# Optimization experiments

Hardware: AMD Instinct MI355X
Metric: run time of the kernel (lower is better)

The kernel has to match this reference:

```python
import jax, jax.numpy as jnp
import numpy as np

B, T, D = 2, 2048, 2048
H, HD, RD = 16, 192, 64
CD = HD - RD          # 128 content dims per head
QR, DL = 768, 512     # q lora rank, kv latent dim
THETA = 10000.0


def setup_inputs() -> dict:
    key = jax.random.key(0)
    ks = jax.random.split(key, 9)
    s = 0.02
    return {
        "x": jax.random.normal(ks[0], (B, T, D), jnp.float32),
        "wq_down": jax.random.normal(ks[1], (D, QR), jnp.float32) * s,
        "wq_up": jax.random.normal(ks[2], (QR, H * CD), jnp.float32) * s,
        "wq_rope": jax.random.normal(ks[3], (D, H * RD), jnp.float32) * s,
        "wkv_down": jax.random.normal(ks[4], (D, DL), jnp.float32) * s,
        "wk_up": jax.random.normal(ks[5], (DL, H * CD), jnp.float32) * s,
        "wv_up": jax.random.normal(ks[6], (DL, H * HD), jnp.float32) * s,
        "wk_rope": jax.random.normal(ks[7], (D, H * RD), jnp.float32) * s,
        "wo": jax.random.normal(ks[8], (H * HD, D), jnp.float32) * s,
    }


def _rope_tables(seq_len):
    inv = 1.0 / (THETA ** (jnp.arange(0, RD, 2, dtype=jnp.float32) / RD))  # [RD/2]
    ang = jnp.arange(seq_len, dtype=jnp.float32)[:, None] * inv[None, :]  # [T, RD/2]
    return jnp.cos(ang), jnp.sin(ang)


def _apply_rope(x, cos, sin):
    # x: [B,H,T,RD]; cos/sin: [T,RD/2] broadcast over B,H
    d = RD // 2
    x1, x2 = x[..., :d], x[..., d:]
    return jnp.concatenate([x1 * cos - x2 * sin, x1 * sin + x2 * cos], axis=-1)


def reference(x, wq_down, wq_up, wq_rope, wkv_down, wk_up, wv_up, wk_rope, wo):
    # projections
    q_c = (x @ wq_down) @ wq_up                       # [B,T,H*CD]
    q_p = x @ wq_rope                                 # [B,T,H*RD]
    latent = x @ wkv_down                             # [B,T,DL]
    k_c = latent @ wk_up                              # [B,T,H*CD]
    k_p = x @ wk_rope                                 # [B,T,H*RD]
    v = latent @ wv_up                                # [B,T,H*HD]

    def heads(t, d):
        return t.reshape(B, T, H, d).transpose(0, 2, 1, 3)  # [B,H,T,d]

    q_c, q_p = heads(q_c, CD), heads(q_p, RD)
    k_c, k_p = heads(k_c, CD), heads(k_p, RD)
    v = heads(v, HD)

    cos, sin = _rope_tables(T)
    q_p = _apply_rope(q_p, cos, sin)
    k_p = _apply_rope(k_p, cos, sin)

    q = jnp.concatenate([q_c, q_p], axis=-1)          # [B,H,T,HD]
    k = jnp.concatenate([k_c, k_p], axis=-1)          # [B,H,T,HD]

    scale = 1.0 / jnp.sqrt(jnp.asarray(HD, q.dtype))
    scores = jnp.einsum("bhqd,bhkd->bhqk", q, k) * scale
    causal = jnp.tril(jnp.ones((T, T), dtype=bool))
    scores = jnp.where(causal, scores, jnp.finfo(scores.dtype).min)
    attn = jax.nn.softmax(scores, axis=-1)
    out = jnp.einsum("bhqk,bhkd->bhqd", attn, v)      # [B,H,T,HD]
    out = out.transpose(0, 2, 1, 3).reshape(B, T, H * HD)
    return out @ wo                                   # [B,T,D]
```

## Files before the change

### kernel.cpp

```cpp
#include <hip/hip_runtime.h>
#include <hip/hip_bf16.h>
#include <cstdint>
#include <cstddef>

typedef __bf16 bf16_t;
typedef __bf16 bf16x8 __attribute__((ext_vector_type(8)));
typedef float f32x4 __attribute__((ext_vector_type(4)));

#define MFMA16(a, b, c) __builtin_amdgcn_mfma_f32_16x16x32_bf16((a), (b), (c), 0, 0, 0)

__device__ __forceinline__ void gload_lds16(const void* g, void* l) {
  __builtin_amdgcn_global_load_lds((__attribute__((address_space(1))) void*)(g),
                                   (__attribute__((address_space(3))) void*)(l),
                                   16, 0, 0);
}

__device__ __forceinline__ uint32_t pkbf(float lo, float hi) {
  union { bf16_t h[2]; uint32_t u; } u2;
  u2.h[0] = (bf16_t)lo; u2.h[1] = (bf16_t)hi;
  return u2.u;
}

__global__ __launch_bounds__(256) void cvt_f32_to_bf16(const float* __restrict__ in,
                                                       bf16_t* __restrict__ out) {
  size_t i = ((size_t)blockIdx.x * 256 + threadIdx.x) * 4;
  float4 v = *(const float4*)(in + i);
  bf16_t o[4] = {(bf16_t)v.x, (bf16_t)v.y, (bf16_t)v.z, (bf16_t)v.w};
  *(uint2*)(out + i) = *(uint2*)o;
}

__global__ __launch_bounds__(256) void transpose_w(const float* __restrict__ in,
                                                   bf16_t* __restrict__ out, int R, int C) {
  __shared__ bf16_t tile[32][33];
  int c0 = blockIdx.x * 32, r0 = blockIdx.y * 32;
  int tx = threadIdx.x, ty = threadIdx.y;
#pragma unroll
  for (int s = 0; s < 4; s++) {
    int r = ty + s * 8;
    tile[r][tx] = (bf16_t)in[(size_t)(r0 + r) * C + c0 + tx];
  }
  __syncthreads();
#pragma unroll
  for (int s = 0; s < 4; s++) {
    int r = ty + s * 8;
    out[(size_t)(c0 + r) * R + r0 + tx] = tile[tx][r];
  }
}

__global__ __launch_bounds__(256) void transpose_v_kernel(const bf16_t* __restrict__ v,
                                                          bf16_t* __restrict__ vt) {
  __shared__ bf16_t tile[32][33];
  int bh = blockIdx.z;
  int t0 = blockIdx.x * 32, d0 = blockIdx.y * 32;
  int tx = threadIdx.x, ty = threadIdx.y;
  const bf16_t* src = v + (size_t)(bh >> 4) * 2048 * 3072 + (bh & 15) * 192;
#pragma unroll
  for (int s = 0; s < 4; s++) {
    int t = ty + s * 8;
    tile[t][tx] = src[(size_t)(t0 + t) * 3072 + d0 + tx];
  }
  __syncthreads();
  bf16_t* dst = vt + (size_t)bh * 192 * 2048;
#pragma unroll
  for (int s = 0; s < 4; s++) {
    int d = ty + s * 8;
    dst[(size_t)(d0 + d) * 2048 + t0 + tx] = tile[tx][d];
  }
}

__global__ __launch_bounds__(256) void rope_inplace(bf16_t* __restrict__ buf) {
  int idx = blockIdx.x * 256 + threadIdx.x;
  int j = idx & 31;
  int h = (idx >> 5) & 15;
  int row = idx >> 9;
  int t = row & 2047;
  size_t base = (size_t)row * 3072 + h * 192 + 128;
  float inv = expf(-(float)j * 0.28782313662425574f);
  float ang = (float)t * inv;
  float c, s;
  sincosf(ang, &s, &c);
  float x1 = (float)buf[base + j];
  float x2 = (float)buf[base + j + 32];
  buf[base + j]      = (bf16_t)(x1 * c - x2 * s);
  buf[base + j + 32] = (bf16_t)(x1 * s + x2 * c);
}

template <int MODE>
__global__ __launch_bounds__(512, 2) void gemm_bt2(const bf16_t* __restrict__ A, int lda,
                                                   const bf16_t* __restrict__ Bt,
                                                   void* __restrict__ C0, void* __restrict__ C1,
                                                   void* __restrict__ C2, int K, int ldc) {
  __shared__ __align__(16) bf16_t sA0[256 * 64];
  __shared__ __align__(16) bf16_t sB0[128 * 64];
  __shared__ __align__(16) bf16_t sA1[256 * 64];
  __shared__ __align__(16) bf16_t sB1[128 * 64];
  const int tid = threadIdx.x;
  const int l = tid & 63, w = tid >> 6;
  const int l15 = l & 15, l4 = (l >> 4) & 3;
  const int wr = w >> 1, wc = w & 1;
  const int m0 = blockIdx.y * 256, n0 = blockIdx.x * 128;
  const int nt = K >> 6;

  f32x4 acc[4][4] = {};

#define STAGEG(SA, SB, KT)                                                          \
  {                                                                                 \
    const int kts = (KT) * 64;                                                      \
    _Pragma("unroll")                                                               \
    for (int r = 0; r < 4; r++) {                                                   \
      int i = r * 512 + tid;                                                        \
      int row = i >> 3, cl = i & 7;                                                 \
      int cg = cl ^ (row & 7);                                                      \
      gload_lds16(A + (size_t)(m0 + row) * lda + kts + cg * 8,                      \
                  (char*)(SA) + (size_t)(r * 512 + w * 64) * 16);                   \
    }                                                                               \
    _Pragma("unroll")                                                               \
    for (int r = 0; r < 2; r++) {                                                   \
      int i = r * 512 + tid;                                                        \
      int row = i >> 3, cl = i & 7;                                                 \
      int cg = cl ^ (row & 7);                                                      \
      gload_lds16(Bt + (size_t)(n0 + row) * K + kts + cg * 8,                       \
                  (char*)(SB) + (size_t)(r * 512 + w * 64) * 16);                   \
    }                                                                               \
  }

#define GCOMPUTE(SA, SB)                                                            \
  {                                                                                 \
    _Pragma("unroll")                                                               \
    for (int ks = 0; ks < 2; ks++) {                                                \
      bf16x8 af[4], bfr[4];                                                         \
      _Pragma("unroll")                                                             \
      for (int mf = 0; mf < 4; mf++) {                                              \
        int row = wr * 64 + mf * 16 + l15;                                          \
        int cl = (ks * 4 + l4) ^ (row & 7);                                         \
        af[mf] = *(const bf16x8*)((SA) + row * 64 + cl * 8);                        \
      }                                                                             \
      _Pragma("unroll")                                                             \
      for (int nf = 0; nf < 4; nf++) {                                              \
        int row = wc * 64 + nf * 16 + l15;                                          \
        int cl = (ks * 4 + l4) ^ (row & 7);                                         \
        bfr[nf] = *(const bf16x8*)((SB) + row * 64 + cl * 8);                       \
      }                                                                             \
      _Pragma("unroll")                                                             \
      for (int mf = 0; mf < 4; mf++)                                                \
        _Pragma("unroll")                                                           \
        for (int nf = 0; nf < 4; nf++)                                              \
          acc[mf][nf] = MFMA16(af[mf], bfr[nf], acc[mf][nf]);                       \
    }                                                                               \
  }

  STAGEG(sA0, sB0, 0)
  for (int t = 0; t < nt; t += 2) {
    STAGEG(sA1, sB1, t + 1)
    asm volatile("s_waitcnt vmcnt(6)\n\ts_barrier" ::: "memory");
    GCOMPUTE(sA0, sB0)
    asm volatile("s_barrier" ::: "memory");
    if (t + 2 < nt) {
      STAGEG(sA0, sB0, t + 2)
      asm volatile("s_waitcnt vmcnt(6)\n\ts_barrier" ::: "memory");
    } else {
      asm volatile("s_waitcnt vmcnt(0)\n\ts_barrier" ::: "memory");
    }
    GCOMPUTE(sA1, sB1)
    asm volatile("s_barrier" ::: "memory");
  }
#undef STAGEG
#undef GCOMPUTE

#pragma unroll
  for (int mf = 0; mf < 4; mf++)
#pragma unroll
    for (int nf = 0; nf < 4; nf++)
#pragma unroll
      for (int r = 0; r < 4; r++) {
        int m = m0 + wr * 64 + mf * 16 + l4 * 4 + r;
        int n = n0 + wc * 64 + nf * 16 + l15;
        float v = acc[mf][nf][r];
        if constexpr (MODE == 1) {
          ((float*)C0)[(size_t)m * ldc + n] = v;
        } else if constexpr (MODE == 2) {
          ((bf16_t*)C0)[(size_t)m * 3072 + (n >> 7) * 192 + (n & 127)] = (bf16_t)v;
        } else if constexpr (MODE == 4) {
          if (n < 1280) {
            ((bf16_t*)C0)[(size_t)m * 1280 + n] = (bf16_t)v;
          } else if (n < 2304) {
            int nn = n - 1280;
            ((bf16_t*)C1)[(size_t)m * 3072 + (nn >> 6) * 192 + 128 + (nn & 63)] = (bf16_t)v;
          } else {
            int nn = n - 2304;
            ((bf16_t*)C2)[(size_t)m * 3072 + (nn >> 6) * 192 + 128 + (nn & 63)] = (bf16_t)v;
          }
        } else {
          if (n < 2048) {
            ((bf16_t*)C0)[(size_t)m * 3072 + (n >> 7) * 192 + (n & 127)] = (bf16_t)v;
          } else {
            ((bf16_t*)C1)[(size_t)m * 3072 + (n - 2048)] = (bf16_t)v;
          }
        }
      }
}

__global__ __launch_bounds__(512, 2) void attn_kernel(const bf16_t* __restrict__ q,
                                                      const bf16_t* __restrict__ kbuf,
                                                      const bf16_t* __restrict__ vt,
                                                      bf16_t* __restrict__ ao) {
  __shared__ __align__(16) bf16_t sK0[64][192];
  __shared__ __align__(16) bf16_t sK1[64][192];
  __shared__ __align__(16) bf16_t sV0[192][64];
  __shared__ __align__(16) bf16_t sV1[192][64];

  const int tid = threadIdx.x, l = tid & 63, w = tid >> 6;
  const int l15 = l & 15, l4 = (l >> 4) & 3;
  const int bh = blockIdx.x & 31;
  const int c = blockIdx.x >> 5;
  const int b = bh >> 4, h = bh & 15;
  const int ca = c, cb = 15 - c;
  const int ra = ca * 128 + w * 16;
  const int rb = cb * 128 + w * 16;
  const int tga = 2 * ca + (w >> 2);
  const int tgb = 2 * cb + (w >> 2);

  const bf16_t* qp = q + (size_t)b * 2048 * 3072 + h * 192;
  const bf16_t* kp = kbuf + (size_t)b * 2048 * 3072 + h * 192;
  const bf16_t* vp = vt + (size_t)bh * 192 * 2048;

  bf16x8 qf[2][6];
#pragma unroll
  for (int kd = 0; kd < 6; kd++) {
    qf[0][kd] = *(const bf16x8*)(qp + (size_t)(ra + l15) * 3072 + kd * 32 + l4 * 8);
    qf[1][kd] = *(const bf16x8*)(qp + (size_t)(rb + l15) * 3072 + kd * 32 + l4 * 8);
  }

  f32x4 o[2][12] = {};
  float mrow[2] = {-__builtin_inff(), -__builtin_inff()};
  float lrow[2] = {0.0f, 0.0f};

  const float scale = 0.07216878364870322f;
  const float THR = 7.0f;
  const int nkt = 2 * cb + 2;
  const int src0 = l15 + ((l4 & 1) << 5);
  const int src1 = src0 + 16;
  const bool hibank = (l4 & 2) != 0;

#define STAGE(SK, SV, KT)                                                           \
  {                                                                                 \
    const int k0s = (KT) * 64;                                                      \
    _Pragma("unroll")                                                               \
    for (int r = 0; r < 3; r++) {                                                   \
      int i = r * 512 + tid;                                                        \
      int row = i / 24, cc = i % 24;                                                \
      int g = cc - (row & 7) * 3;                                                   \
      if (g < 0) g += 24;                                                           \
      gload_lds16(kp + (size_t)(k0s + row) * 3072 + g * 8,                          \
                  (char*)&SK[0][0] + (size_t)(r * 512 + w * 64) * 16);              \
    }                                                                               \
    _Pragma("unroll")                                                               \
    for (int r = 0; r < 3; r++) {                                                   \
      int i = r * 512 + tid;                                                        \
      int d = i >> 3, cc = i & 7;                                                   \
      gload_lds16(vp + (size_t)d * 2048 + k0s + (cc ^ (d & 7)) * 8,                 \
                  (char*)&SV[0][0] + (size_t)(r * 512 + w * 64) * 16);              \
    }                                                                               \
  }

#define SOFTMAX_CHUNK(c, rbase, tg)                                                    \
    {                                                                                  \
      const bool diag = (kt == (tg));                                                  \
      _Pragma("unroll")                                                                \
      for (int nf = 0; nf < 4; nf++)                                                   \
        _Pragma("unroll")                                                              \
        for (int r = 0; r < 4; r++) {                                                  \
          float sv = s[c][nf][r] * scale;                                              \
          if (diag) {                                                                  \
            int ktok = k0 + nf * 16 + l4 * 4 + r;                                      \
            if (ktok > (rbase) + l15) sv = -__builtin_inff();                          \
          }                                                                            \
          s[c][nf][r] = sv;                                                            \
        }                                                                              \
      float m_in = s[c][0][0];                                                         \
      _Pragma("unroll")                                                                \
      for (int nf = 0; nf < 4; nf++)                                                   \
        _Pragma("unroll")                                                              \
        for (int r = 0; r < 4; r++)                                                    \
          if (nf | r) m_in = fmaxf(m_in, s[c][nf][r]);                                 \
      m_in = fmaxf(m_in, __shfl_xor(m_in, 16));                                        \
      m_in = fmaxf(m_in, __shfl_xor(m_in, 32));                                        \
      if (!__all(m_in - mrow[c] <= THR)) {                                             \
        float mn = fmaxf(mrow[c], m_in);                                               \
        float alpha = __expf(mrow[c] - mn);                                            \
        mrow[c] = mn;                                                                  \
        lrow[c] *= alpha;                                                              \
        f32x4 av;                                                                      \
        _Pragma("unroll")                                                              \
        for (int r = 0; r < 4; r++) av[r] = __shfl(alpha, l4 * 4 + r);                 \
        _Pragma("unroll")                                                              \
        for (int nf2 = 0; nf2 < 12; nf2++) o[c][nf2] *= av;                            \
      }                                                                                \
      float rs = 0.0f;                                                                 \
      _Pragma("unroll")                                                                \
      for (int nf = 0; nf < 4; nf++)                                                   \
        _Pragma("unroll")                                                              \
        for (int r = 0; r < 4; r++) {                                                  \
          float pv = __expf(s[c][nf][r] - mrow[c]);                                    \
          s[c][nf][r] = pv;                                                            \
          rs += pv;                                                                    \
        }                                                                              \
      rs += __shfl_xor(rs, 16);                                                        \
      rs += __shfl_xor(rs, 32);                                                        \
      lrow[c] += rs;                                                                   \
      uint32_t wq[8];                                                                  \
      _Pragma("unroll")                                                                \
      for (int nf = 0; nf < 4; nf++) {                                                 \
        wq[nf * 2 + 0] = pkbf(s[c][nf][0], s[c][nf][1]);                               \
        wq[nf * 2 + 1] = pkbf(s[c][nf][2], s[c][nf][3]);                               \
      }                                                                                \
      _Pragma("unroll")                                                                \
      for (int ks = 0; ks < 2; ks++) {                                                 \
        uint32_t A0 = __shfl(wq[(2 * ks) * 2 + 0], src0);                              \
        uint32_t A1 = __shfl(wq[(2 * ks) * 2 + 1], src0);                              \
        uint32_t B0 = __shfl(wq[(2 * ks + 1) * 2 + 0], src0);                          \
        uint32_t B1 = __shfl(wq[(2 * ks + 1) * 2 + 1], src0);                          \
        uint32_t C0w = __shfl(wq[(2 * ks) * 2 + 0], src1);                             \
        uint32_t C1w = __shfl(wq[(2 * ks) * 2 + 1], src1);                             \
        uint32_t D0 = __shfl(wq[(2 * ks + 1) * 2 + 0], src1);                          \
        uint32_t D1 = __shfl(wq[(2 * ks + 1) * 2 + 1], src1);                          \
        union { uint32_t u[4]; bf16x8 v; } fr;                                         \
        fr.u[0] = hibank ? B0 : A0;                                                    \
        fr.u[1] = hibank ? B1 : A1;                                                    \
        fr.u[2] = hibank ? D0 : C0w;                                                   \
        fr.u[3] = hibank ? D1 : C1w;                                                   \
        pa[c][ks] = fr.v;                                                              \
      }                                                                                \
    }

#define TILE_BODY(SK, SV, KT)                                                          \
  {                                                                                    \
    const int kt = (KT);                                                               \
    const int k0 = kt * 64;                                                            \
    const bool act_a = (kt <= tga);                                                    \
    const bool act_b = (kt <= tgb);                                                    \
    f32x4 s[2][4] = {};                                                                \
    _Pragma("unroll")                                                                  \
    for (int kd = 0; kd < 6; kd++) {                                                   \
      bf16x8 bk[4];                                                                    \
      _Pragma("unroll")                                                                \
      for (int nf = 0; nf < 4; nf++) {                                                 \
        int row = nf * 16 + l15;                                                       \
        int cl = kd * 4 + l4 + (row & 7) * 3;                                          \
        if (cl >= 24) cl -= 24;                                                        \
        bk[nf] = *(const bf16x8*)(&SK[row][cl * 8]);                                   \
      }                                                                                \
      if (act_b) {                                                                     \
        _Pragma("unroll")                                                              \
        for (int nf = 0; nf < 4; nf++)                                                 \
          s[1][nf] = MFMA16(bk[nf], qf[1][kd], s[1][nf]);                              \
      }                                                                                \
      if (act_a) {                                                                     \
        _Pragma("unroll")                                                              \
        for (int nf = 0; nf < 4; nf++)                                                 \
          s[0][nf] = MFMA16(bk[nf], qf[0][kd], s[0][nf]);                              \
      }                                                                                \
    }                                                                                  \
    bf16x8 pa[2][2] = {};                                                              \
    if (act_b) SOFTMAX_CHUNK(1, rb, tgb)                                               \
    if (act_a) SOFTMAX_CHUNK(0, ra, tga)                                               \
    _Pragma("unroll")                                                                  \
    for (int ks = 0; ks < 2; ks++) {                                                   \
      _Pragma("unroll")                                                                \
      for (int nf2 = 0; nf2 < 12; nf2++) {                                             \
        int d = nf2 * 16 + l15;                                                        \
        int cl = (ks * 4 + l4) ^ (d & 7);                                              \
        bf16x8 vb = *(const bf16x8*)(&SV[d][cl * 8]);                                  \
        if (act_b) o[1][nf2] = MFMA16(pa[1][ks], vb, o[1][nf2]);                       \
        if (act_a) o[0][nf2] = MFMA16(pa[0][ks], vb, o[0][nf2]);                       \
      }                                                                                \
    }                                                                                  \
  }

  STAGE(sK0, sV0, 0)
  __syncthreads();

  for (int kt0 = 0; kt0 < nkt; kt0 += 2) {
    STAGE(sK1, sV1, kt0 + 1)
    TILE_BODY(sK0, sV0, kt0)
    __syncthreads();
    if (kt0 + 2 < nkt) STAGE(sK0, sV0, kt0 + 2)
    TILE_BODY(sK1, sV1, kt0 + 1)
    __syncthreads();
  }
#undef STAGE
#undef SOFTMAX_CHUNK
#undef TILE_BODY

#pragma unroll
  for (int mf = 0; mf < 2; mf++) {
    const int rbase = (mf == 0) ? ra : rb;
#pragma unroll
    for (int r = 0; r < 4; r++) {
      float lv = __shfl(lrow[mf], l4 * 4 + r);
      float inv = 1.0f / lv;
      int qrow = rbase + l4 * 4 + r;
#pragma unroll
      for (int nf2 = 0; nf2 < 12; nf2++) {
        int d = nf2 * 16 + l15;
        ao[(size_t)(b * 2048 + qrow) * 3072 + h * 192 + d] = (bf16_t)(o[mf][nf2][r] * inv);
      }
    }
  }
}

extern "C" void kernel_launch(void* const* d_in, const int* in_sizes, int n_in,
                              void* d_out, int out_size, void* d_ws, size_t ws_size,
                              hipStream_t stream) {
  const float* x       = (const float*)d_in[0];
  const float* wq_down = (const float*)d_in[1];
  const float* wq_up   = (const float*)d_in[2];
  const float* wq_rope = (const float*)d_in[3];
  const float* wkv_down= (const float*)d_in[4];
  const float* wk_up   = (const float*)d_in[5];
  const float* wv_up   = (const float*)d_in[6];
  const float* wk_rope = (const float*)d_in[7];
  const float* wo      = (const float*)d_in[8];
  float* out = (float*)d_out;

  char* p = (char*)d_ws;
  auto take = [&](size_t elems) { bf16_t* r = (bf16_t*)p; p += elems * 2; return r; };
  bf16_t* xb    = take(4096ull * 2048);
  bf16_t* fw1   = take(3328ull * 2048);
  bf16_t* wqu_t = take(2048ull * 768);
  bf16_t* fw2   = take(5120ull * 512);
  bf16_t* wo_t  = take(2048ull * 3072);
  bf16_t* qkvd  = take(4096ull * 1280);
  bf16_t* qbuf  = take(4096ull * 3072);
  bf16_t* kbuf  = take(4096ull * 3072);
  bf16_t* vbuf  = take(4096ull * 3072);
  bf16_t* vt    = take(4096ull * 3072);
  bf16_t* ao    = vbuf;

  dim3 tb(32, 8);
  cvt_f32_to_bf16<<<8192, 256, 0, stream>>>(x, xb);
  transpose_w<<<dim3(24, 64), tb, 0, stream>>>(wq_down,  fw1,                 2048, 768);
  transpose_w<<<dim3(16, 64), tb, 0, stream>>>(wkv_down, fw1 + 768ull * 2048, 2048, 512);
  transpose_w<<<dim3(32, 64), tb, 0, stream>>>(wq_rope,  fw1 + 1280ull * 2048,2048, 1024);
  transpose_w<<<dim3(32, 64), tb, 0, stream>>>(wk_rope,  fw1 + 2304ull * 2048,2048, 1024);
  transpose_w<<<dim3(64, 24), tb, 0, stream>>>(wq_up,    wqu_t,               768, 2048);
  transpose_w<<<dim3(64, 16), tb, 0, stream>>>(wk_up,    fw2,                 512, 2048);
  transpose_w<<<dim3(96, 16), tb, 0, stream>>>(wv_up,    fw2 + 2048ull * 512, 512, 3072);
  transpose_w<<<dim3(64, 96), tb, 0, stream>>>(wo,       wo_t,                3072, 2048);

  gemm_bt2<4><<<dim3(26, 16), 512, 0, stream>>>(xb, 2048, fw1, qkvd, qbuf, kbuf, 2048, 0);
  gemm_bt2<2><<<dim3(16, 16), 512, 0, stream>>>(qkvd, 1280, wqu_t, qbuf, nullptr, nullptr, 768, 0);
  gemm_bt2<5><<<dim3(40, 16), 512, 0, stream>>>(qkvd + 768, 1280, fw2, kbuf, vbuf, nullptr, 512, 0);

  rope_inplace<<<8192, 256, 0, stream>>>(qbuf);
  rope_inplace<<<8192, 256, 0, stream>>>(kbuf);
  transpose_v_kernel<<<dim3(64, 6, 32), tb, 0, stream>>>(vbuf, vt);

  attn_kernel<<<256, 512, 0, stream>>>(qbuf, kbuf, vt, ao);

  gemm_bt2<1><<<dim3(16, 16), 512, 0, stream>>>(ao, 3072, wo_t, out, nullptr, nullptr, 3072, 2048);
}
```

Measured before the change: 373.3 us.

## Fuse weight transposes, rope launches, and write V transposed from GEMM epilogue

Merges the eight weight-transpose launches into one flat-grid kernel and the two rope launches into one. The K/V up-projection GEMM epilogue now writes V directly in per-head transposed layout using packed 4-element stores, which removes the separate V transpose kernel and its extra pass over V. This cuts launch overhead and memory traffic. The trade-off is a more complex epilogue with strided stores across the T dimension.

```diff
diff --git a/kernel.cpp b/kernel.cpp
--- a/kernel.cpp
+++ b/kernel.cpp
@@ -29,47 +29,45 @@
   *(uint2*)(out + i) = *(uint2*)o;
 }
 
-__global__ __launch_bounds__(256) void transpose_w(const float* __restrict__ in,
-                                                   bf16_t* __restrict__ out, int R, int C) {
+__global__ __launch_bounds__(256) void transpose_all(
+    const float* __restrict__ s0, const float* __restrict__ s1,
+    const float* __restrict__ s2, const float* __restrict__ s3,
+    const float* __restrict__ s4, const float* __restrict__ s5,
+    const float* __restrict__ s6, const float* __restrict__ s7,
+    bf16_t* __restrict__ t0, bf16_t* __restrict__ t1, bf16_t* __restrict__ t2,
+    bf16_t* __restrict__ t3, bf16_t* __restrict__ t4, bf16_t* __restrict__ t5,
+    bf16_t* __restrict__ t6, bf16_t* __restrict__ t7) {
   __shared__ bf16_t tile[32][33];
-  int c0 = blockIdx.x * 32, r0 = blockIdx.y * 32;
-  int tx = threadIdx.x, ty = threadIdx.y;
+  const int lid = blockIdx.x;
+  const float* src; bf16_t* dst; int R, C, bx, by;
+  if (lid < 1536)       { src=s0; dst=t0; R=2048; C=768;  int lo=lid;        bx=lo%24; by=lo/24; }
+  else if (lid < 2560)  { src=s1; dst=t1; R=2048; C=512;  int lo=lid-1536;   bx=lo%16; by=lo/16; }
+  else if (lid < 4608)  { src=s2; dst=t2; R=2048; C=1024; int lo=lid-2560;   bx=lo%32; by=lo/32; }
+  else if (lid < 6656)  { src=s3; dst=t3; R=2048; C=1024; int lo=lid-4608;   bx=lo%32; by=lo/32; }
+  else if (lid < 8192)  { src=s4; dst=t4; R=768;  C=2048; int lo=lid-6656;   bx=lo%64; by=lo/64; }
+  else if (lid < 9216)  { src=s5; dst=t5; R=512;  C=2048; int lo=lid-8192;   bx=lo%64; by=lo/64; }
+  else if (lid < 10752) { src=s6; dst=t6; R=512;  C=3072; int lo=lid-9216;   bx=lo%96; by=lo/96; }
+  else                  { src=s7; dst=t7; R=3072; C=2048; int lo=lid-10752;  bx=lo%64; by=lo/64; }
+  const int c0 = bx * 32, r0 = by * 32;
+  const int tx = threadIdx.x, ty = threadIdx.y;
 #pragma unroll
   for (int s = 0; s < 4; s++) {
     int r = ty + s * 8;
-    tile[r][tx] = (bf16_t)in[(size_t)(r0 + r) * C + c0 + tx];
+    tile[r][tx] = (bf16_t)src[(size_t)(r0 + r) * C + c0 + tx];
   }
   __syncthreads();
 #pragma unroll
   for (int s = 0; s < 4; s++) {
     int r = ty + s * 8;
-    out[(size_t)(c0 + r) * R + r0 + tx] = tile[tx][r];
-  }
-}
-
-__global__ __launch_bounds__(256) void transpose_v_kernel(const bf16_t* __restrict__ v,
-                                                          bf16_t* __restrict__ vt) {
-  __shared__ bf16_t tile[32][33];
-  int bh = blockIdx.z;
-  int t0 = blockIdx.x * 32, d0 = blockIdx.y * 32;
-  int tx = threadIdx.x, ty = threadIdx.y;
-  const bf16_t* src = v + (size_t)(bh >> 4) * 2048 * 3072 + (bh & 15) * 192;
-#pragma unroll
-  for (int s = 0; s < 4; s++) {
-    int t = ty + s * 8;
-    tile[t][tx] = src[(size_t)(t0 + t) * 3072 + d0 + tx];
-  }
-  __syncthreads();
-  bf16_t* dst = vt + (size_t)bh * 192 * 2048;
-#pragma unroll
-  for (int s = 0; s < 4; s++) {
-    int d = ty + s * 8;
-    dst[(size_t)(d0 + d) * 2048 + t0 + tx] = tile[tx][d];
-  }
-}
-
-__global__ __launch_bounds__(256) void rope_inplace(bf16_t* __restrict__ buf) {
-  int idx = blockIdx.x * 256 + threadIdx.x;
+    dst[(size_t)(c0 + r) * R + r0 + tx] = tile[tx][r];
+  }
+}
+
+__global__ __launch_bounds__(256) void rope_both(bf16_t* __restrict__ qb,
+                                                 bf16_t* __restrict__ kb) {
+  const int gid = blockIdx.x;
+  bf16_t* buf = (gid < 8192) ? qb : kb;
+  int idx = (gid & 8191) * 256 + threadIdx.x;
   int j = idx & 31;
   int h = (idx >> 5) & 15;
   int row = idx >> 9;
@@ -170,34 +168,53 @@
 #pragma unroll
   for (int mf = 0; mf < 4; mf++)
 #pragma unroll
-    for (int nf = 0; nf < 4; nf++)
-#pragma unroll
-      for (int r = 0; r < 4; r++) {
-        int m = m0 + wr * 64 + mf * 16 + l4 * 4 + r;
-        int n = n0 + wc * 64 + nf * 16 + l15;
-        float v = acc[mf][nf][r];
-        if constexpr (MODE == 1) {
-          ((float*)C0)[(size_t)m * ldc + n] = v;
-        } else if constexpr (MODE == 2) {
-          ((bf16_t*)C0)[(size_t)m * 3072 + (n >> 7) * 192 + (n & 127)] = (bf16_t)v;
-        } else if constexpr (MODE == 4) {
-          if (n < 1280) {
-            ((bf16_t*)C0)[(size_t)m * 1280 + n] = (bf16_t)v;
-          } else if (n < 2304) {
-            int nn = n - 1280;
-            ((bf16_t*)C1)[(size_t)m * 3072 + (nn >> 6) * 192 + 128 + (nn & 63)] = (bf16_t)v;
-          } else {
-            int nn = n - 2304;
-            ((bf16_t*)C2)[(size_t)m * 3072 + (nn >> 6) * 192 + 128 + (nn & 63)] = (bf16_t)v;
-          }
+    for (int nf = 0; nf < 4; nf++) {
+      const int mbase = m0 + wr * 64 + mf * 16 + l4 * 4;
+      const int n = n0 + wc * 64 + nf * 16 + l15;
+      if constexpr (MODE == 1) {
+#pragma unroll
+        for (int r = 0; r < 4; r++)
+          ((float*)C0)[(size_t)(mbase + r) * ldc + n] = acc[mf][nf][r];
+      } else if constexpr (MODE == 2) {
+#pragma unroll
+        for (int r = 0; r < 4; r++)
+          ((bf16_t*)C0)[(size_t)(mbase + r) * 3072 + (n >> 7) * 192 + (n & 127)] =
+              (bf16_t)acc[mf][nf][r];
+      } else if constexpr (MODE == 4) {
+        if (n < 1280) {
+#pragma unroll
+          for (int r = 0; r < 4; r++)
+            ((bf16_t*)C0)[(size_t)(mbase + r) * 1280 + n] = (bf16_t)acc[mf][nf][r];
+        } else if (n < 2304) {
+          int nn = n - 1280;
+#pragma unroll
+          for (int r = 0; r < 4; r++)
+            ((bf16_t*)C1)[(size_t)(mbase + r) * 3072 + (nn >> 6) * 192 + 128 + (nn & 63)] =
+                (bf16_t)acc[mf][nf][r];
         } else {
-          if (n < 2048) {
-            ((bf16_t*)C0)[(size_t)m * 3072 + (n >> 7) * 192 + (n & 127)] = (bf16_t)v;
-          } else {
-            ((bf16_t*)C1)[(size_t)m * 3072 + (n - 2048)] = (bf16_t)v;
-          }
+          int nn = n - 2304;
+#pragma unroll
+          for (int r = 0; r < 4; r++)
+            ((bf16_t*)C2)[(size_t)(mbase + r) * 3072 + (nn >> 6) * 192 + 128 + (nn & 63)] =
+                (bf16_t)acc[mf][nf][r];
+        }
+      } else {
+        if (n < 2048) {
+#pragma unroll
+          for (int r = 0; r < 4; r++)
+            ((bf16_t*)C0)[(size_t)(mbase + r) * 3072 + (n >> 7) * 192 + (n & 127)] =
+                (bf16_t)acc[mf][nf][r];
+        } else {
+          int nn = n - 2048;
+          int hh = nn / 192, dd = nn - hh * 192;
+          int bb = mbase >> 11, tt = mbase & 2047;
+          bf16_t pk4[4] = {(bf16_t)acc[mf][nf][0], (bf16_t)acc[mf][nf][1],
+                           (bf16_t)acc[mf][nf][2], (bf16_t)acc[mf][nf][3]};
+          *(uint2*)((bf16_t*)C1 + ((size_t)(bb * 16 + hh) * 192 + dd) * 2048 + tt) =
+              *(uint2*)pk4;
         }
       }
+    }
 }
 
 __global__ __launch_bounds__(512, 2) void attn_kernel(const bf16_t* __restrict__ q,
@@ -433,28 +450,21 @@
   bf16_t* qkvd  = take(4096ull * 1280);
   bf16_t* qbuf  = take(4096ull * 3072);
   bf16_t* kbuf  = take(4096ull * 3072);
-  bf16_t* vbuf  = take(4096ull * 3072);
+  bf16_t* ao    = take(4096ull * 3072);
   bf16_t* vt    = take(4096ull * 3072);
-  bf16_t* ao    = vbuf;
 
   dim3 tb(32, 8);
   cvt_f32_to_bf16<<<8192, 256, 0, stream>>>(x, xb);
-  transpose_w<<<dim3(24, 64), tb, 0, stream>>>(wq_down,  fw1,                 2048, 768);
-  transpose_w<<<dim3(16, 64), tb, 0, stream>>>(wkv_down, fw1 + 768ull * 2048, 2048, 512);
-  transpose_w<<<dim3(32, 64), tb, 0, stream>>>(wq_rope,  fw1 + 1280ull * 2048,2048, 1024);
-  transpose_w<<<dim3(32, 64), tb, 0, stream>>>(wk_rope,  fw1 + 2304ull * 2048,2048, 1024);
-  transpose_w<<<dim3(64, 24), tb, 0, stream>>>(wq_up,    wqu_t,               768, 2048);
-  transpose_w<<<dim3(64, 16), tb, 0, stream>>>(wk_up,    fw2,                 512, 2048);
-  transpose_w<<<dim3(96, 16), tb, 0, stream>>>(wv_up,    fw2 + 2048ull * 512, 512, 3072);
-  transpose_w<<<dim3(64, 96), tb, 0, stream>>>(wo,       wo_t,                3072, 2048);
+  transpose_all<<<16896, tb, 0, stream>>>(
+      wq_down, wkv_down, wq_rope, wk_rope, wq_up, wk_up, wv_up, wo,
+      fw1, fw1 + 768ull * 2048, fw1 + 1280ull * 2048, fw1 + 2304ull * 2048,
+      wqu_t, fw2, fw2 + 2048ull * 512, wo_t);
 
   gemm_bt2<4><<<dim3(26, 16), 512, 0, stream>>>(xb, 2048, fw1, qkvd, qbuf, kbuf, 2048, 0);
   gemm_bt2<2><<<dim3(16, 16), 512, 0, stream>>>(qkvd, 1280, wqu_t, qbuf, nullptr, nullptr, 768, 0);
-  gemm_bt2<5><<<dim3(40, 16), 512, 0, stream>>>(qkvd + 768, 1280, fw2, kbuf, vbuf, nullptr, 512, 0);
-
-  rope_inplace<<<8192, 256, 0, stream>>>(qbuf);
-  rope_inplace<<<8192, 256, 0, stream>>>(kbuf);
-  transpose_v_kernel<<<dim3(64, 6, 32), tb, 0, stream>>>(vbuf, vt);
+  gemm_bt2<5><<<dim3(40, 16), 512, 0, stream>>>(qkvd + 768, 1280, fw2, kbuf, vt, nullptr, 512, 0);
+
+  rope_both<<<16384, 256, 0, stream>>>(qbuf, kbuf);
 
   attn_kernel<<<256, 512, 0, stream>>>(qbuf, kbuf, vt, ao);
 
```

Result: faster. 347.1 us (-7.0%).
